# Performance work log

Hardware: AMD Instinct MI355X
Metric: run time of the kernel (lower is better)

The kernel has to match this reference:

```python
import jax, jax.numpy as jnp
import numpy as np

N = 100000
E = 1000000
IN_C = 256
HID = 64
OUT = 64
NEG_SLOPE = 0.2


def setup_inputs() -> dict:
    key = jax.random.key(0)
    ks = jax.random.split(key, 12)
    x = jax.random.normal(ks[0], (N, IN_C), dtype=jnp.float32)
    edge_index = jax.random.randint(ks[1], (2, E), 0, N, dtype=jnp.int64)
    s = 1.0 / np.sqrt(IN_C)
    W1 = jax.random.uniform(ks[2], (IN_C, HID), jnp.float32, -s, s)
    a1_src = jax.random.uniform(ks[3], (HID,), jnp.float32, -s, s)
    a1_dst = jax.random.uniform(ks[4], (HID,), jnp.float32, -s, s)
    b1 = jnp.zeros((HID,), jnp.float32)
    s2 = 1.0 / np.sqrt(HID)
    W2 = jax.random.uniform(ks[5], (HID, OUT), jnp.float32, -s2, s2)
    a2_src = jax.random.uniform(ks[6], (OUT,), jnp.float32, -s2, s2)
    a2_dst = jax.random.uniform(ks[7], (OUT,), jnp.float32, -s2, s2)
    b2 = jnp.zeros((OUT,), jnp.float32)
    return {"x": x, "edge_index": edge_index, "W1": W1, "a1_src": a1_src,
            "a1_dst": a1_dst, "b1": b1, "W2": W2, "a2_src": a2_src,
            "a2_dst": a2_dst, "b2": b2}


def gat_conv(x, W, a_src, a_dst, b, src, dst):
    h = x @ W                              # [N, d]
    alpha_s = h @ a_src                    # [N]
    alpha_d = h @ a_dst                    # [N]
    e = jax.nn.leaky_relu(alpha_s[src] + alpha_d[dst], NEG_SLOPE)  # [E]
    # segment softmax over incoming edges of each destination node
    e_max = jax.lax.stop_gradient(jax.ops.segment_max(e, dst, num_segments=N))
    ex = jnp.exp(e - e_max[dst])
    denom = jax.ops.segment_sum(ex, dst, num_segments=N)
    alpha = ex / (denom[dst] + 1e-16)      # [E]
    out = jax.ops.segment_sum(alpha[:, None] * h[src], dst, num_segments=N)
    return out + b


def reference(x, edge_index, W1, a1_src, a1_dst, b1, W2, a2_src, a2_dst, b2):
    src, dst = edge_index[0], edge_index[1]
    # dropout(p=0.6) is identity in eval mode
    h = jax.nn.relu(gat_conv(x, W1, a1_src, a1_dst, b1, src, dst))
    out = gat_conv(h, W2, a2_src, a2_dst, b2, src, dst)
    return out
```

## Files before the change

kernel.cpp:

```cpp
#include <hip/hip_runtime.h>
#include <math.h>

#define HID 64
#define BSH 9
#define NPB 512
#define EPB 4096
#define CAP 8192

typedef __attribute__((ext_vector_type(8))) short bf16x8;
typedef __attribute__((ext_vector_type(4))) float f32x4;
typedef __attribute__((ext_vector_type(4))) unsigned int u32x4;

__device__ __forceinline__ unsigned short f2bf(float f) {
    unsigned u = __float_as_uint(f);
    unsigned r = u + 0x7FFF + ((u >> 16) & 1);
    return (unsigned short)(r >> 16);
}
__device__ __forceinline__ float bf2f(unsigned short b) {
    return __uint_as_float(((unsigned)b) << 16);
}


__global__ __launch_bounds__(256) void bucket_scatter(const int* __restrict__ esrc,
                                                      const int* __restrict__ edst,
                                                      int* __restrict__ bcnt,
                                                      int* __restrict__ ebuf, int E_, int NB) {
    __shared__ int hist[256], chunk[256], lcur[256];
    int t = threadIdx.x;
    hist[t] = 0;
    lcur[t] = 0;
    __syncthreads();
    int base = blockIdx.x * EPB;
    int s[EPB / 256], d[EPB / 256];
#pragma unroll
    for (int r = 0; r < EPB / 256; ++r) {
        int i = base + r * 256 + t;
        if (i < E_) {
            s[r] = esrc[i];
            d[r] = edst[i];
            atomicAdd(&hist[d[r] >> BSH], 1);
        } else {
            d[r] = -1;
        }
    }
    __syncthreads();
    if (t < NB) chunk[t] = hist[t] ? atomicAdd(&bcnt[t], hist[t]) : 0;
    __syncthreads();
#pragma unroll
    for (int r = 0; r < EPB / 256; ++r) {
        if (d[r] >= 0) {
            int b = d[r] >> BSH;
            int pos = chunk[b] + atomicAdd(&lcur[b], 1);
            ebuf[b * CAP + pos] = (s[r] << BSH) | (d[r] & (NPB - 1));
        }
    }
}

__global__ __launch_bounds__(256) void csr_build(const int* __restrict__ ebuf,
                                                 const int* __restrict__ bcnt,
                                                 int2* __restrict__ offs,
                                                 int* __restrict__ srcs, int Nv) {
    __shared__ int dhist[NPB], dbase[NPB], psum[256];
    int b = blockIdx.x, t = threadIdx.x;
    int cnt = bcnt[b];
    int e0 = b * CAP;
#pragma unroll
    for (int j = t; j < NPB; j += 256) dhist[j] = 0;
    __syncthreads();
    for (int i = t; i < cnt; i += 256) {
        atomicAdd(&dhist[ebuf[e0 + i] & (NPB - 1)], 1);
    }
    __syncthreads();
    int a0 = dhist[2 * t], a1 = dhist[2 * t + 1];
    psum[t] = a0 + a1;
    __syncthreads();
    for (int o = 1; o < 256; o <<= 1) {
        int u = (t >= o) ? psum[t - o] : 0;
        __syncthreads();
        psum[t] += u;
        __syncthreads();
    }
    int ex = psum[t] - (a0 + a1);
    dbase[2 * t] = ex;
    dbase[2 * t + 1] = ex + a0;
    __syncthreads();
#pragma unroll
    for (int j = t; j < NPB; j += 256) {
        int node = (b << BSH) + j;
        if (node < Nv) {
            int beg = e0 + dbase[j];
            offs[node] = make_int2(beg, beg + dhist[j]);
        }
    }
    __syncthreads();
    for (int i = t; i < cnt; i += 256) {
        int e = ebuf[e0 + i];
        int pos = atomicAdd(&dbase[e & (NPB - 1)], 1);
        srcs[e0 + pos] = e >> BSH;
    }
}


__global__ __launch_bounds__(256) void wt_kernel(const float* __restrict__ W1,
                                                 const float* __restrict__ W2,
                                                 unsigned short* __restrict__ Wt1,
                                                 unsigned short* __restrict__ Wt2) {
    int t = threadIdx.x;
    int blk = blockIdx.x;
    int n = t & 63;
    if (blk < 64) {
        int k = blk * 4 + (t >> 6);
        Wt1[(size_t)n * 256 + k] = f2bf(W1[(size_t)k * 64 + n]);
    } else {
        int k = (blk - 64) * 4 + (t >> 6);
        Wt2[(size_t)n * 64 + k] = f2bf(W2[(size_t)k * 64 + n]);
    }
}


template <int K, bool BF16IN>
__global__ __launch_bounds__(256) void gemm_mfma(const void* __restrict__ Xv,
                                                 const unsigned short* __restrict__ Wt,
                                                 const float* __restrict__ a_s,
                                                 const float* __restrict__ a_d,
                                                 unsigned short* __restrict__ C,
                                                 float* __restrict__ as_,
                                                 float* __restrict__ ad_, int Nrows) {
    constexpr int KPAD = K + 8;
    constexpr int XPAD = 72;
    __shared__ __align__(16) unsigned short Ws[64 * KPAD];
    __shared__ __align__(16) unsigned short Xs[128 * XPAD];

    const float* Xf = (const float*)Xv;
    const unsigned short* Xb = (const unsigned short*)Xv;

    int t = threadIdx.x;
    int n0 = blockIdx.x * 128;
    int lane = t & 63;
    int w = t >> 6;
    int m = lane & 15;
    int q = lane >> 4;
    int base = n0 + w * 32;

    constexpr int KC8 = K / 8;
    for (int i = t; i < 64 * KC8; i += 256) {
        int n = i / KC8;
        int kc = i % KC8;
        u32x4 v = *(const u32x4*)(Wt + (size_t)n * K + kc * 8);
        *(u32x4*)(&Ws[n * KPAD + kc * 8]) = v;
    }

    f32x4 acc[2][4];
#pragma unroll
    for (int mi = 0; mi < 2; ++mi)
#pragma unroll
        for (int ct = 0; ct < 4; ++ct) acc[mi][ct] = (f32x4){0.f, 0.f, 0.f, 0.f};

    for (int k0 = 0; k0 < K; k0 += 64) {
        if (!BF16IN) {
#pragma unroll
            for (int i = 0; i < 8; ++i) {
                int idx = i * 256 + t;
                int row = idx >> 4;
                int kq = (idx & 15) * 4;
                int gn = n0 + row;
                if (gn >= Nrows) gn = Nrows - 1;
                float4 v = *(const float4*)(Xf + (size_t)gn * K + k0 + kq);
                ushort4 bb;
                bb.x = f2bf(v.x); bb.y = f2bf(v.y); bb.z = f2bf(v.z); bb.w = f2bf(v.w);
                *(ushort4*)(&Xs[row * XPAD + kq]) = bb;
            }
        } else {
#pragma unroll
            for (int i = 0; i < 4; ++i) {
                int idx = i * 256 + t;
                int row = idx >> 3;
                int kq = (idx & 7) * 8;
                int gn = n0 + row;
                if (gn >= Nrows) gn = Nrows - 1;
                u32x4 v = *(const u32x4*)(Xb + (size_t)gn * K + k0 + kq);
                *(u32x4*)(&Xs[row * XPAD + kq]) = v;
            }
        }
        __syncthreads();
#pragma unroll
        for (int ks = 0; ks < 64; ks += 32) {
            bf16x8 a0 = *(const bf16x8*)(&Xs[(w * 32 + m) * XPAD + ks + q * 8]);
            bf16x8 a1 = *(const bf16x8*)(&Xs[(w * 32 + 16 + m) * XPAD + ks + q * 8]);
#pragma unroll
            for (int ct = 0; ct < 4; ++ct) {
                bf16x8 bv = *(const bf16x8*)(&Ws[(ct * 16 + m) * KPAD + k0 + ks + q * 8]);
                acc[0][ct] = __builtin_amdgcn_mfma_f32_16x16x32_bf16(a0, bv, acc[0][ct], 0, 0, 0);
                acc[1][ct] = __builtin_amdgcn_mfma_f32_16x16x32_bf16(a1, bv, acc[1][ct], 0, 0, 0);
            }
        }
        __syncthreads();
    }

    float sa0 = a_s[m], sa1 = a_s[16 + m], sa2 = a_s[32 + m], sa3 = a_s[48 + m];
    float da0 = a_d[m], da1 = a_d[16 + m], da2 = a_d[32 + m], da3 = a_d[48 + m];

#pragma unroll
    for (int mi = 0; mi < 2; ++mi) {
#pragma unroll
        for (int r = 0; r < 4; ++r) {
            int row = base + mi * 16 + q * 4 + r;
            if (row < Nrows) {
                size_t ro = (size_t)row * 64 + m;
                C[ro]      = f2bf(acc[mi][0][r]);
                C[ro + 16] = f2bf(acc[mi][1][r]);
                C[ro + 32] = f2bf(acc[mi][2][r]);
                C[ro + 48] = f2bf(acc[mi][3][r]);
            }
        }
        float vs[4], vd[4];
#pragma unroll
        for (int r = 0; r < 4; ++r) {
            float s = acc[mi][0][r] * sa0 + acc[mi][1][r] * sa1 +
                      acc[mi][2][r] * sa2 + acc[mi][3][r] * sa3;
            float d = acc[mi][0][r] * da0 + acc[mi][1][r] * da1 +
                      acc[mi][2][r] * da2 + acc[mi][3][r] * da3;
#pragma unroll
            for (int o = 1; o < 16; o <<= 1) {
                s += __shfl_xor(s, o);
                d += __shfl_xor(d, o);
            }
            vs[r] = s;
            vd[r] = d;
        }
        if (m < 4) {
            int row = base + mi * 16 + q * 4 + m;
            float wvs = (m == 0) ? vs[0] : (m == 1) ? vs[1] : (m == 2) ? vs[2] : vs[3];
            float wvd = (m == 0) ? vd[0] : (m == 1) ? vd[1] : (m == 2) ? vd[2] : vd[3];
            if (row < Nrows) {
                as_[row] = wvs;
                ad_[row] = wvd;
            }
        }
    }
}


template <bool RELU_BF16OUT>
__global__ __launch_bounds__(256) void agg_kernel(const unsigned short* __restrict__ H,
                                                  const float* __restrict__ as_,
                                                  const float* __restrict__ ad_,
                                                  const float* __restrict__ bias,
                                                  const int2* __restrict__ offs,
                                                  const int* __restrict__ srcs,
                                                  void* __restrict__ outp, int Nrows) {
    int d = blockIdx.x * 4 + (threadIdx.x >> 6);
    int lane = threadIdx.x & 63;
    if (d >= Nrows) return;
    int2 oe = offs[d];
    int begin = oe.x, end = oe.y;
    float adv = ad_[d];
    float acc = 0.f, lsum = 0.f;

    for (int bbase = begin; bbase < end; bbase += 64) {
        int cnt = end - bbase;
        if (cnt > 64) cnt = 64;
        int s = 0;
        float p = 0.f;
        if (lane < cnt) {
            s = srcs[bbase + lane];
            float x = as_[s] + adv;
            x = (x > 0.f) ? x : 0.2f * x;
            p = __expf(x);
        }
        lsum += p;
        int nb = (cnt + 7) & ~7;
        for (int j = 0; j < nb; j += 8) {
            float hv[8], pv[8];
#pragma unroll
            for (int u = 0; u < 8; ++u) {
                int su = __builtin_amdgcn_readlane(s, j + u);
                pv[u] = __uint_as_float(
                    (unsigned)__builtin_amdgcn_readlane((int)__float_as_uint(p), j + u));
                hv[u] = bf2f(H[(size_t)su * HID + lane]);
            }
#pragma unroll
            for (int u = 0; u < 8; ++u) acc += pv[u] * hv[u];
        }
    }
#pragma unroll
    for (int o = 32; o; o >>= 1) lsum += __shfl_xor(lsum, o);
    float o = acc / (lsum + 1e-16f) + bias[lane];
    if (RELU_BF16OUT) {
        ((unsigned short*)outp)[(size_t)d * HID + lane] = f2bf(fmaxf(o, 0.f));
    } else {
        ((float*)outp)[(size_t)d * HID + lane] = o;
    }
}


extern "C" void kernel_launch(void* const* d_in, const int* in_sizes, int n_in,
                              void* d_out, int out_size, void* d_ws, size_t ws_size,
                              hipStream_t stream) {
    const float* x      = (const float*)d_in[0];
    const int*   edge   = (const int*)d_in[1];
    const float* W1     = (const float*)d_in[2];
    const float* a1_src = (const float*)d_in[3];
    const float* a1_dst = (const float*)d_in[4];
    const float* b1     = (const float*)d_in[5];
    const float* W2     = (const float*)d_in[6];
    const float* a2_src = (const float*)d_in[7];
    const float* a2_dst = (const float*)d_in[8];
    const float* b2     = (const float*)d_in[9];
    float* out = (float*)d_out;

    const int N = in_sizes[0] / 256;
    const int E = in_sizes[1] / 2;
    const int IN_C = 256;
    const int NB = (N + NPB - 1) >> BSH;

    char* w = (char*)d_ws;
    auto alloc = [&](size_t bytes) {
        char* p = w;
        w += (bytes + 255) & ~(size_t)255;
        return p;
    };
    int2*           offs  = (int2*)alloc((size_t)N * 8);
    int*            srcs  = (int*)alloc((size_t)NB * CAP * 4);
    int*            ebuf  = (int*)alloc((size_t)NB * CAP * 4);
    int*            bcnt  = (int*)alloc(256 * 4);
    unsigned short* h1    = (unsigned short*)alloc((size_t)N * HID * 2);
    unsigned short* hB    = (unsigned short*)alloc((size_t)N * HID * 2);
    float*          as_   = (float*)alloc((size_t)N * 4);
    float*          ad_   = (float*)alloc((size_t)N * 4);
    unsigned short* Wt1   = (unsigned short*)alloc((size_t)IN_C * 64 * 2);
    unsigned short* Wt2   = (unsigned short*)alloc((size_t)64 * 64 * 2);

    const int* esrc = edge;
    const int* edst = edge + E;

    hipMemsetAsync(bcnt, 0, 256 * 4, stream);

    wt_kernel<<<IN_C / 4 + 64 / 4, 256, 0, stream>>>(W1, W2, Wt1, Wt2);

    int gbk = (E + EPB - 1) / EPB;
    bucket_scatter<<<gbk, 256, 0, stream>>>(esrc, edst, bcnt, ebuf, E, NB);
    csr_build<<<NB, 256, 0, stream>>>(ebuf, bcnt, offs, srcs, N);

    int gblocks = (N + 127) / 128;
    int ablocks = (N + 3) / 4;

    gemm_mfma<256, false><<<gblocks, 256, 0, stream>>>(x, Wt1, a1_src, a1_dst, h1, as_, ad_, N);
    agg_kernel<true><<<ablocks, 256, 0, stream>>>(h1, as_, ad_, b1, offs, srcs, hB, N);

    gemm_mfma<64, true><<<gblocks, 256, 0, stream>>>(hB, Wt2, a2_src, a2_dst, h1, as_, ad_, N);
    agg_kernel<false><<<ablocks, 256, 0, stream>>>(h1, as_, ad_, b2, offs, srcs, out, N);
}
```

Before: 316.2 us.

## Gather four edges per wave with 8-byte row loads in GAT aggregation

The aggregation kernel now splits each 64-lane wave into four 16-lane groups. Each group handles a different edge and loads 4 bf16 features per lane as one 8-byte load, and the partial sums are combined with cross-group shuffles at the end. This replaces the per-lane 2-byte gathers and the readlane broadcasts with wider loads that keep more edges in flight. The memset of the bucket counters is also folded into the weight-transpose kernel, which drops one launch.

```diff
diff --git a/kernel.cpp b/kernel.cpp
--- a/kernel.cpp
+++ b/kernel.cpp
@@ -10,6 +10,7 @@
 typedef __attribute__((ext_vector_type(8))) short bf16x8;
 typedef __attribute__((ext_vector_type(4))) float f32x4;
 typedef __attribute__((ext_vector_type(4))) unsigned int u32x4;
+typedef __attribute__((ext_vector_type(2))) unsigned int u32x2;
 
 __device__ __forceinline__ unsigned short f2bf(float f) {
     unsigned u = __float_as_uint(f);
@@ -104,10 +105,12 @@
 __global__ __launch_bounds__(256) void wt_kernel(const float* __restrict__ W1,
                                                  const float* __restrict__ W2,
                                                  unsigned short* __restrict__ Wt1,
-                                                 unsigned short* __restrict__ Wt2) {
+                                                 unsigned short* __restrict__ Wt2,
+                                                 int* __restrict__ bcnt) {
     int t = threadIdx.x;
     int blk = blockIdx.x;
     int n = t & 63;
+    if (blk == 0) bcnt[t] = 0;
     if (blk < 64) {
         int k = blk * 4 + (t >> 6);
         Wt1[(size_t)n * 256 + k] = f2bf(W1[(size_t)k * 64 + n]);
@@ -255,7 +258,11 @@
     int2 oe = offs[d];
     int begin = oe.x, end = oe.y;
     float adv = ad_[d];
-    float acc = 0.f, lsum = 0.f;
+    float lsum = 0.f;
+    float a0 = 0.f, a1 = 0.f, a2 = 0.f, a3 = 0.f;
+    int g4 = lane >> 4;
+    int hq = lane & 15;
+    const unsigned short* Hq = H + (size_t)hq * 4;
 
     for (int bbase = begin; bbase < end; bbase += 64) {
         int cnt = end - bbase;
@@ -269,27 +276,49 @@
             p = __expf(x);
         }
         lsum += p;
-        int nb = (cnt + 7) & ~7;
-        for (int j = 0; j < nb; j += 8) {
-            float hv[8], pv[8];
-#pragma unroll
-            for (int u = 0; u < 8; ++u) {
-                int su = __builtin_amdgcn_readlane(s, j + u);
-                pv[u] = __uint_as_float(
-                    (unsigned)__builtin_amdgcn_readlane((int)__float_as_uint(p), j + u));
-                hv[u] = bf2f(H[(size_t)su * HID + lane]);
-            }
-#pragma unroll
-            for (int u = 0; u < 8; ++u) acc += pv[u] * hv[u];
-        }
+        int nb = (cnt + 3) & ~3;
+        for (int j = 0; j < nb; j += 4) {
+            int e = j + g4;
+            int su = __shfl(s, e);
+            float pu = __shfl(p, e);
+            u32x2 hv = *(const u32x2*)(Hq + (size_t)su * HID);
+            float h0 = __uint_as_float(hv.x << 16);
+            float h1 = __uint_as_float(hv.x & 0xFFFF0000u);
+            float h2 = __uint_as_float(hv.y << 16);
+            float h3 = __uint_as_float(hv.y & 0xFFFF0000u);
+            a0 += pu * h0;
+            a1 += pu * h1;
+            a2 += pu * h2;
+            a3 += pu * h3;
+        }
+    }
+#pragma unroll
+    for (int o = 16; o <= 32; o <<= 1) {
+        a0 += __shfl_xor(a0, o);
+        a1 += __shfl_xor(a1, o);
+        a2 += __shfl_xor(a2, o);
+        a3 += __shfl_xor(a3, o);
     }
 #pragma unroll
     for (int o = 32; o; o >>= 1) lsum += __shfl_xor(lsum, o);
-    float o = acc / (lsum + 1e-16f) + bias[lane];
-    if (RELU_BF16OUT) {
-        ((unsigned short*)outp)[(size_t)d * HID + lane] = f2bf(fmaxf(o, 0.f));
-    } else {
-        ((float*)outp)[(size_t)d * HID + lane] = o;
+    float inv = 1.f / (lsum + 1e-16f);
+    if (g4 == 0) {
+        float4 bv = *(const float4*)(bias + hq * 4);
+        float o0 = a0 * inv + bv.x;
+        float o1 = a1 * inv + bv.y;
+        float o2 = a2 * inv + bv.z;
+        float o3 = a3 * inv + bv.w;
+        if (RELU_BF16OUT) {
+            ushort4 ov;
+            ov.x = f2bf(fmaxf(o0, 0.f));
+            ov.y = f2bf(fmaxf(o1, 0.f));
+            ov.z = f2bf(fmaxf(o2, 0.f));
+            ov.w = f2bf(fmaxf(o3, 0.f));
+            *(ushort4*)((unsigned short*)outp + (size_t)d * HID + hq * 4) = ov;
+        } else {
+            *(float4*)((float*)outp + (size_t)d * HID + hq * 4) =
+                make_float4(o0, o1, o2, o3);
+        }
     }
 }
 
@@ -334,9 +363,7 @@
     const int* esrc = edge;
     const int* edst = edge + E;
 
-    hipMemsetAsync(bcnt, 0, 256 * 4, stream);
-
-    wt_kernel<<<IN_C / 4 + 64 / 4, 256, 0, stream>>>(W1, W2, Wt1, Wt2);
+    wt_kernel<<<IN_C / 4 + 64 / 4, 256, 0, stream>>>(W1, W2, Wt1, Wt2, bcnt);
 
     int gbk = (E + EPB - 1) / EPB;
     bucket_scatter<<<gbk, 256, 0, stream>>>(esrc, edst, bcnt, ebuf, E, NB);
```

Result: no change. 322.3 us (+1.9%).
